# Performance work log

Hardware: AMD Instinct MI355X
Metric: run time of the kernel (lower is better)

The kernel has to match this reference:

```python
import jax, jax.numpy as jnp
import numpy as np

N = 65536      # n query/support points
NN = 34        # neighbors per point
K = 15         # kernel points
IN_F = 64
OUT_F = 64
RADIUS = 2.5
KP_EXTENT_CFG = 1.0
DENSITY = 5.0
EXTENT = KP_EXTENT_CFG * RADIUS / DENSITY  # effective KP_extent = 0.5
BN_EPS = 1e-6
LRELU_SLOPE = 0.1
POINT_DIM = 4  # modulated=True -> 3 offset dims + 1 modulation per kernel point


def make_kernel_points():
    # Deterministic stand-in for the precomputed kernel dispositions loaded
    # from disk in KPConv (fixed='center': first point at origin). Points lie
    # inside a ball of radius 1.5 * extent.
    rng = np.random.RandomState(42)
    kp = rng.normal(size=(K, 3))
    kp /= np.linalg.norm(kp, axis=1, keepdims=True)
    kp *= rng.uniform(0.3, 1.0, size=(K, 1))
    kp[0] = 0.0
    return jnp.asarray(kp * (1.5 * EXTENT), dtype=jnp.float32)


def setup_inputs() -> dict:
    key = jax.random.key(0)
    ks = jax.random.split(key, 8)
    query_points = jax.random.uniform(ks[0], (N, 3), dtype=jnp.float32)
    support_points = jax.random.uniform(ks[1], (N, 3), dtype=jnp.float32)
    neighbors_indices = jax.random.randint(ks[2], (N, NN), 0, N, dtype=jnp.int32)
    features = jax.random.normal(ks[3], (N, IN_F), dtype=jnp.float32)
    # weight_variable: truncated normal with std sqrt(2/size[-1])
    weight = jax.random.truncated_normal(ks[4], -2.0, 2.0, (K, IN_F, OUT_F), jnp.float32) * np.sqrt(2.0 / OUT_F)
    off_dim = POINT_DIM * K
    offset_weight = jax.random.truncated_normal(ks[5], -2.0, 2.0, (K, IN_F, off_dim), jnp.float32) * np.sqrt(2.0 / off_dim)
    offset_bias = jnp.zeros((off_dim,), jnp.float32)
    bn_gamma = jnp.ones((OUT_F,), jnp.float32)
    bn_beta = jnp.zeros((OUT_F,), jnp.float32)
    kernel_points = make_kernel_points()
    return dict(query_points=query_points, support_points=support_points,
                neighbors_indices=neighbors_indices, features=features,
                weight=weight, offset_weight=offset_weight, offset_bias=offset_bias,
                bn_gamma=bn_gamma, bn_beta=bn_beta, kernel_points=kernel_points)


def _influence(sq_dist):
    # KP_influence='linear': relu(1 - d / extent)
    return jax.nn.relu(1.0 - jnp.sqrt(sq_dist) / EXTENT)


def reference(query_points, support_points, neighbors_indices, features,
              weight, offset_weight, offset_bias, bn_gamma, bn_beta, kernel_points):
    n = query_points.shape[0]
    # Shadow point (far away) / shadow feature (zeros) appended at index n0
    supp_pad = jnp.concatenate([support_points, jnp.full((1, 3), 1e6, jnp.float32)], 0)
    feat_pad = jnp.concatenate([features, jnp.zeros((1, IN_F), jnp.float32)], 0)

    neigh_pts = supp_pad[neighbors_indices] - query_points[:, None, :]   # [n,nn,3]
    neigh_feats = feat_pad[neighbors_indices]                            # [n,nn,in]

    # ---- rigid KPConv producing per-point offsets (+ modulations) ----
    sq0 = jnp.sum((neigh_pts[:, :, None, :] - kernel_points[None, None]) ** 2, -1)  # [n,nn,K]
    w0 = _influence(sq0)
    wf0 = jnp.einsum('nak,nac->nkc', w0, neigh_feats)                    # [n,K,in]
    f0 = jnp.einsum('nkc,kcd->nd', wf0, offset_weight) + offset_bias     # [n,4K]
    offsets = f0[:, :3 * K].reshape(n, K, 3) * EXTENT                    # rescale to layer extent
    modulations = 2.0 * jax.nn.sigmoid(f0[:, 3 * K:])                    # [n,K]

    # ---- deformable KPConv ----
    def_kp = kernel_points[None] + offsets                               # [n,K,3]
    sq = jnp.sum((neigh_pts[:, :, None, :] - def_kp[:, None, :, :]) ** 2, -1)  # [n,nn,K]
    w = _influence(sq)                                                   # aggregation_mode='sum'
    wf = jnp.einsum('nak,nac->nkc', w, neigh_feats) * modulations[:, :, None]
    x = jnp.einsum('nkc,kco->no', wf, weight)                            # [n,out]

    # BatchNorm1d (training-mode batch stats, eps=1e-6) + LeakyReLU(0.1)
    mean = x.mean(0)
    var = x.var(0)
    x = (x - mean) * jax.lax.rsqrt(var + BN_EPS) * bn_gamma + bn_beta
    return jnp.where(x >= 0, x, LRELU_SLOPE * x)
```

## Files before the change

### kernel.cpp

```cpp
#include <hip/hip_runtime.h>
#include <math.h>

#define NPTS 65536

using half8   = __attribute__((ext_vector_type(8))) _Float16;
using half4   = __attribute__((ext_vector_type(4))) _Float16;
using floatx4 = __attribute__((ext_vector_type(4))) float;

__global__ __launch_bounds__(256) void k_prep(
    const float* __restrict__ ow, const float* __restrict__ w,
    const float* __restrict__ feat,
    _Float16* __restrict__ owt, _Float16* __restrict__ wt,
    _Float16* __restrict__ featH, float* __restrict__ stats)
{
  int b = blockIdx.x;
  if (b < 64) {
    __shared__ float tile[256][9];
    int mat = b >> 5, bb = b & 31;
    int kcb = bb & 3, db = bb >> 2;
    int t = threadIdx.x;
    int kc = kcb * 256 + t;
    int c = kc >> 4, k = kc & 15;
    const float* src = mat ? w : ow;
    int dmax = mat ? 64 : 60;
    #pragma unroll
    for (int di = 0; di < 8; ++di) {
      int d = db * 8 + di;
      float v = 0.f;
      if (k < 15 && d < dmax) v = src[(k * 64 + c) * dmax + d];
      tile[t][di] = v;
    }
    __syncthreads();
    _Float16* dst = mat ? wt : owt;
    int k2 = t >> 5, lo = t & 31;
    #pragma unroll
    for (int di = 0; di < 8; ++di) {
      int d = db * 8 + di;
      int wv = d >> 4, mm = d & 15;
      dst[((wv * 4 + kcb) * 8 + k2) * 512 + mm * 32 + lo] = (_Float16)tile[t][di];
    }
    if (b == 0 && t < 128) stats[t] = 0.f;
  } else {
    int j = (b - 64) * 256 + threadIdx.x;
    float4 f = ((const float4*)feat)[j];
    half4 h = {(_Float16)f.x, (_Float16)f.y, (_Float16)f.z, (_Float16)f.w};
    ((half4*)featH)[j] = h;
  }
}

__global__ __launch_bounds__(256, 4) void k_fused(
    const float* __restrict__ query, const float* __restrict__ support,
    const int* __restrict__ nidx, const _Float16* __restrict__ featH,
    const float* __restrict__ kpts, const float* __restrict__ obias,
    const _Float16* __restrict__ owt, const _Float16* __restrict__ wt,
    float* __restrict__ outx, float* __restrict__ stats)
{
  __shared__ float                  npx[16][34], npy[16][34], npz[16][34];
  __shared__ unsigned short         sidx[16][34];
  __shared__ __align__(16) _Float16 fT[4][64 * 32];
  __shared__ unsigned int           fx2s[16][64];
  __shared__ __align__(16) _Float16 wfh[16 * 264];
  __shared__ float                  dk[16][60];

  const int tid  = threadIdx.x;
  const int wave = tid >> 6, lane = tid & 63;
  const int quad = lane >> 4, mm = lane & 15;
  const int base = blockIdx.x * 16;
  _Float16* fTw = fT[wave];
  unsigned int* fTw32 = (unsigned int*)fTw;
  const floatx4 fz = {0.f, 0.f, 0.f, 0.f};
  const int me = (mm < 15) ? mm : 14;
  const int mmw = (mm & 6) | ((mm & 1) << 3) | ((mm >> 3) & 1);

  for (int s = tid; s < 544; s += 256) {
    int pt = s / 34, a = s - pt * 34;
    int n = base + pt;
    int id = nidx[n * 34 + a];
    npx[pt][a] = support[id * 3 + 0] - query[n * 3 + 0];
    npy[pt][a] = support[id * 3 + 1] - query[n * 3 + 1];
    npz[pt][a] = support[id * 3 + 2] - query[n * 3 + 2];
    sidx[pt][a] = (unsigned short)id;
  }
  __syncthreads();

  if (tid < 128) {
    int pt = tid >> 3, ch = tid & 7;
    int i0 = (int)sidx[pt][32], i1 = (int)sidx[pt][33];
    uint4 g0 = *(const uint4*)(featH + i0 * 64 + ch * 8);
    uint4 g1 = *(const uint4*)(featH + i1 * 64 + ch * 8);
    const uint* p0 = (const uint*)&g0;
    const uint* p1 = (const uint*)&g1;
    #pragma unroll
    for (int cc = 0; cc < 8; ++cc) {
      uint v = __builtin_amdgcn_perm(p1[cc >> 1], p0[cc >> 1],
                                     (cc & 1) ? 0x07060302u : 0x05040100u);
      fx2s[pt][ch * 8 + cc] = v;
    }
  }
  __syncthreads();

  auto load_g = [&](int pl, uint4* g0, uint4* g1) {
    #pragma unroll
    for (int it = 0; it < 2; ++it) {
      int task = it * 64 + lane;
      int rp = task >> 3, ch = task & 7;
      int i0 = (int)sidx[pl][2 * rp], i1 = (int)sidx[pl][2 * rp + 1];
      g0[it] = *(const uint4*)(featH + i0 * 64 + ch * 8);
      g1[it] = *(const uint4*)(featH + i1 * 64 + ch * 8);
    }
  };
  auto transpose_g = [&](const uint4* g0, const uint4* g1) {
    #pragma unroll
    for (int it = 0; it < 2; ++it) {
      int task = it * 64 + lane;
      int rp = task >> 3, ch = task & 7;
      int chunk = rp >> 2, o = rp & 3;
      const uint* p0 = (const uint*)&g0[it];
      const uint* p1 = (const uint*)&g1[it];
      #pragma unroll
      for (int cc = 0; cc < 8; ++cc) {
        int c  = ch * 8 + cc;
        int fc = (c & 0x36) | ((c & 1) << 3) | ((c >> 3) & 1);
        int pc = chunk ^ ((ch ^ cc) & 3);
        uint v = __builtin_amdgcn_perm(p1[cc >> 1], p0[cc >> 1],
                                       (cc & 1) ? 0x07060302u : 0x05040100u);
        fTw32[fc * 16 + pc * 4 + o] = v;
      }
    }
  };

  auto conv_point = [&](int pl, float kx, float ky, float kz, float modme,
                        half4* hq3) {
    half8 a0;
    #pragma unroll
    for (int j = 0; j < 8; ++j) {
      int a = quad * 8 + j;
      float dx = npx[pl][a] - kx, dy = npy[pl][a] - ky, dz = npz[pl][a] - kz;
      float wv = 1.f - 2.f * sqrtf(dx * dx + dy * dy + dz * dz);
      a0[j] = (_Float16)(fmaxf(wv, 0.f) * modme);
    }
    float dx = npx[pl][32] - kx, dy = npy[pl][32] - ky, dz = npz[pl][32] - kz;
    float w32 = fmaxf(1.f - 2.f * sqrtf(dx * dx + dy * dy + dz * dz), 0.f) * modme;
    dx = npx[pl][33] - kx; dy = npy[pl][33] - ky; dz = npz[pl][33] - kz;
    float w33 = fmaxf(1.f - 2.f * sqrtf(dx * dx + dy * dy + dz * dz), 0.f) * modme;
    half8 a2 = {};
    a2[0] = (_Float16)((quad == 0) ? w32 : 0.f);
    a2[1] = (_Float16)((quad == 0) ? w33 : 0.f);
    #pragma unroll
    for (int ct = 0; ct < 4; ++ct) {
      int c  = ct * 16 + mmw;
      int pc = quad ^ (((c >> 3) ^ c) & 3);
      half8 b = *(const half8*)(fTw + (ct * 16 + mm) * 32 + pc * 8);
      floatx4 acc = __builtin_amdgcn_mfma_f32_16x16x32_f16(a0, b, fz, 0, 0, 0);
      uint fp = fx2s[pl][c];
      half8 b2 = {};
      b2[0] = __builtin_bit_cast(_Float16, (unsigned short)(fp & 0xffffu));
      b2[1] = __builtin_bit_cast(_Float16, (unsigned short)(fp >> 16));
      acc = __builtin_amdgcn_mfma_f32_16x16x32_f16(a2, b2, acc, 0, 0, 0);
      half4 h = {(_Float16)acc[0], (_Float16)acc[1],
                 (_Float16)acc[2], (_Float16)acc[3]};
      if (ct == 0) *(half4*)(wfh + pl * 264 + mmw * 16 + quad * 4) = h;
      else         hq3[ct - 1] = h;
    }
  };

  auto write_hold = [&](const half4 (*hq)[3], int idx) {
    #pragma unroll
    for (int pp = 0; pp < 4; ++pp)
      *(half4*)(wfh + (wave * 4 + pp) * 264 + mmw * 16 + quad * 4) = hq[pp][idx];
  };

  auto gemm_q = [&](const _Float16* bmat, int p, floatx4& A, floatx4& B) {
    const _Float16* brow = bmat + ((wave * 4 + p) * 8) * 512 + mm * 32 + quad * 8;
    const _Float16* arow = wfh + mm * 264;
    #pragma unroll
    for (int k2 = 0; k2 < 8; ++k2) {
      half8 af = *(const half8*)(arow + k2 * 32 + quad * 8);
      half8 bf = *(const half8*)(brow + k2 * 512);
      if (k2 & 1) B = __builtin_amdgcn_mfma_f32_16x16x32_f16(af, bf, B, 0, 0, 0);
      else        A = __builtin_amdgcn_mfma_f32_16x16x32_f16(af, bf, A, 0, 0, 0);
    }
  };

  uint4 G0[2], G1[2];
  half4 hq[4][3];
  const float k0x = kpts[me * 3 + 0], k0y = kpts[me * 3 + 1], k0z = kpts[me * 3 + 2];

  {
    load_g(wave * 4, G0, G1);
    #pragma unroll
    for (int pp = 0; pp < 4; ++pp) {
      int pl = wave * 4 + pp;
      transpose_g(G0, G1);
      if (pp < 3) load_g(pl + 1, G0, G1);
      conv_point(pl, k0x, k0y, k0z, 1.f, hq[pp]);
    }
  }
  load_g(wave * 4, G0, G1);
  __syncthreads();

  {
    floatx4 A = fz, B = fz;
    gemm_q(owt, 0, A, B);
    __syncthreads(); write_hold(hq, 0); __syncthreads();
    gemm_q(owt, 1, A, B);
    __syncthreads(); write_hold(hq, 1); __syncthreads();
    gemm_q(owt, 2, A, B);
    __syncthreads(); write_hold(hq, 2); __syncthreads();
    gemm_q(owt, 3, A, B);
    int d = wave * 16 + mm;
    float bv = (d < 60) ? obias[d] : 0.f;
    float kv = (d < 45) ? kpts[d] : 0.f;
    #pragma unroll
    for (int r = 0; r < 4; ++r) {
      int pt = quad * 4 + r;
      float v = A[r] + B[r] + bv;
      if (d < 60)
        dk[pt][d] = (d < 45) ? (kv + 0.5f * v)
                             : (2.f / (1.f + expf(-v)));
    }
  }
  __syncthreads();

  #pragma unroll
  for (int pp = 0; pp < 4; ++pp) {
    int pl = wave * 4 + pp;
    float kx = dk[pl][me * 3 + 0], ky = dk[pl][me * 3 + 1], kz = dk[pl][me * 3 + 2];
    float modme = dk[pl][45 + me];
    transpose_g(G0, G1);
    if (pp < 3) load_g(pl + 1, G0, G1);
    conv_point(pl, kx, ky, kz, modme, hq[pp]);
  }
  __syncthreads();

  {
    floatx4 A = fz, B = fz;
    gemm_q(wt, 0, A, B);
    __syncthreads(); write_hold(hq, 0); __syncthreads();
    gemm_q(wt, 1, A, B);
    __syncthreads(); write_hold(hq, 1); __syncthreads();
    gemm_q(wt, 2, A, B);
    __syncthreads(); write_hold(hq, 2); __syncthreads();
    gemm_q(wt, 3, A, B);
    int d = wave * 16 + mm;
    float s1 = 0.f, s2 = 0.f;
    #pragma unroll
    for (int r = 0; r < 4; ++r) {
      float v = A[r] + B[r];
      outx[(base + quad * 4 + r) * 64 + d] = v;
      s1 += v; s2 += v * v;
    }
    s1 += __shfl_xor(s1, 16); s2 += __shfl_xor(s2, 16);
    s1 += __shfl_xor(s1, 32); s2 += __shfl_xor(s2, 32);
    if (lane < 16) {
      atomicAdd(&stats[d], s1);
      atomicAdd(&stats[64 + d], s2);
    }
  }
}

__global__ __launch_bounds__(256) void k_norm(
    float* __restrict__ x, const float* __restrict__ stats,
    const float* __restrict__ gamma, const float* __restrict__ beta)
{
  const int i = blockIdx.x * 256 + threadIdx.x;
  float4 v = ((float4*)x)[i];
  const int c0 = (i * 4) & 63;
  float o[4] = {v.x, v.y, v.z, v.w};
  #pragma unroll
  for (int j = 0; j < 4; ++j) {
    int c = c0 + j;
    float mean = stats[c] * (1.f / NPTS);
    float var  = stats[64 + c] * (1.f / NPTS) - mean * mean;
    float s = rsqrtf(var + 1e-6f) * gamma[c];
    float y = (o[j] - mean) * s + beta[c];
    o[j] = (y >= 0.f) ? y : 0.1f * y;
  }
  float4 rv = {o[0], o[1], o[2], o[3]};
  ((float4*)x)[i] = rv;
}

extern "C" void kernel_launch(void* const* d_in, const int* in_sizes, int n_in,
                              void* d_out, int out_size, void* d_ws, size_t ws_size,
                              hipStream_t stream)
{
  const float* query   = (const float*)d_in[0];
  const float* support = (const float*)d_in[1];
  const int*   nidx    = (const int*)d_in[2];
  const float* feat    = (const float*)d_in[3];
  const float* weight  = (const float*)d_in[4];
  const float* oweight = (const float*)d_in[5];
  const float* obias   = (const float*)d_in[6];
  const float* gamma   = (const float*)d_in[7];
  const float* beta    = (const float*)d_in[8];
  const float* kpts    = (const float*)d_in[9];
  float* x = (float*)d_out;

  char* ws = (char*)d_ws;
  _Float16* featH = (_Float16*)ws;
  _Float16* owt   = (_Float16*)(ws + 8388608);
  _Float16* wt    = (_Float16*)(ws + 8519680);
  float*    stats = (float*)(ws + 8650752);

  k_prep<<<4160, 256, 0, stream>>>(oweight, weight, feat, owt, wt, featH, stats);
  k_fused<<<4096, 256, 0, stream>>>(query, support, nidx, featH, kpts, obias,
                                    owt, wt, x, stats);
  k_norm<<<4096, 256, 0, stream>>>(x, stats, gamma, beta);
}
```

Baseline: 257.0 us.

## Pack neighbor offsets as float4 with squared norm and expand distance algebraically

Neighbor offsets now go into one float4 array that also holds the precomputed squared norm. Kernel-point distances are computed as |p|^2+|k|^2-2p·k, which replaces per-pair subtractions with a dot product and turns three LDS reads into one vector read. The deformed kernel points and modulations are stored in fp16 in shared memory, and the MFMA loops in gemm_q raise wave priority with s_setprio. The expanded form risks cancellation error and the fp16 offsets lose precision, though the distance is clamped at zero.

```diff
diff --git a/kernel.cpp b/kernel.cpp
--- a/kernel.cpp
+++ b/kernel.cpp
@@ -55,12 +55,12 @@
     const _Float16* __restrict__ owt, const _Float16* __restrict__ wt,
     float* __restrict__ outx, float* __restrict__ stats)
 {
-  __shared__ float                  npx[16][34], npy[16][34], npz[16][34];
+  __shared__ float4                 np4[16][34];
   __shared__ unsigned short         sidx[16][34];
   __shared__ __align__(16) _Float16 fT[4][64 * 32];
   __shared__ unsigned int           fx2s[16][64];
   __shared__ __align__(16) _Float16 wfh[16 * 264];
-  __shared__ float                  dk[16][60];
+  __shared__ _Float16               dkh[16][60];
 
   const int tid  = threadIdx.x;
   const int wave = tid >> 6, lane = tid & 63;
@@ -76,9 +76,11 @@
     int pt = s / 34, a = s - pt * 34;
     int n = base + pt;
     int id = nidx[n * 34 + a];
-    npx[pt][a] = support[id * 3 + 0] - query[n * 3 + 0];
-    npy[pt][a] = support[id * 3 + 1] - query[n * 3 + 1];
-    npz[pt][a] = support[id * 3 + 2] - query[n * 3 + 2];
+    float dx = support[id * 3 + 0] - query[n * 3 + 0];
+    float dy = support[id * 3 + 1] - query[n * 3 + 1];
+    float dz = support[id * 3 + 2] - query[n * 3 + 2];
+    float4 q = {dx, dy, dz, dx * dx + dy * dy + dz * dz};
+    np4[pt][a] = q;
     sidx[pt][a] = (unsigned short)id;
   }
   __syncthreads();
@@ -131,18 +133,22 @@
 
   auto conv_point = [&](int pl, float kx, float ky, float kz, float modme,
                         half4* hq3) {
+    float hk = kx * kx + ky * ky + kz * kz;
     half8 a0;
     #pragma unroll
     for (int j = 0; j < 8; ++j) {
       int a = quad * 8 + j;
-      float dx = npx[pl][a] - kx, dy = npy[pl][a] - ky, dz = npz[pl][a] - kz;
-      float wv = 1.f - 2.f * sqrtf(dx * dx + dy * dy + dz * dz);
-      a0[j] = (_Float16)(fmaxf(wv, 0.f) * modme);
-    }
-    float dx = npx[pl][32] - kx, dy = npy[pl][32] - ky, dz = npz[pl][32] - kz;
-    float w32 = fmaxf(1.f - 2.f * sqrtf(dx * dx + dy * dy + dz * dz), 0.f) * modme;
-    dx = npx[pl][33] - kx; dy = npy[pl][33] - ky; dz = npz[pl][33] - kz;
-    float w33 = fmaxf(1.f - 2.f * sqrtf(dx * dx + dy * dy + dz * dz), 0.f) * modme;
+      float4 q = np4[pl][a];
+      float dt = q.x * kx + q.y * ky + q.z * kz;
+      float d2 = fmaxf(q.w + hk - 2.f * dt, 0.f);
+      a0[j] = (_Float16)(fmaxf(1.f - 2.f * sqrtf(d2), 0.f) * modme);
+    }
+    float4 q = np4[pl][32];
+    float dt = q.x * kx + q.y * ky + q.z * kz;
+    float w32 = fmaxf(1.f - 2.f * sqrtf(fmaxf(q.w + hk - 2.f * dt, 0.f)), 0.f) * modme;
+    q = np4[pl][33];
+    dt = q.x * kx + q.y * ky + q.z * kz;
+    float w33 = fmaxf(1.f - 2.f * sqrtf(fmaxf(q.w + hk - 2.f * dt, 0.f)), 0.f) * modme;
     half8 a2 = {};
     a2[0] = (_Float16)((quad == 0) ? w32 : 0.f);
     a2[1] = (_Float16)((quad == 0) ? w33 : 0.f);
@@ -173,6 +179,7 @@
   auto gemm_q = [&](const _Float16* bmat, int p, floatx4& A, floatx4& B) {
     const _Float16* brow = bmat + ((wave * 4 + p) * 8) * 512 + mm * 32 + quad * 8;
     const _Float16* arow = wfh + mm * 264;
+    __builtin_amdgcn_s_setprio(1);
     #pragma unroll
     for (int k2 = 0; k2 < 8; ++k2) {
       half8 af = *(const half8*)(arow + k2 * 32 + quad * 8);
@@ -180,6 +187,7 @@
       if (k2 & 1) B = __builtin_amdgcn_mfma_f32_16x16x32_f16(af, bf, B, 0, 0, 0);
       else        A = __builtin_amdgcn_mfma_f32_16x16x32_f16(af, bf, A, 0, 0, 0);
     }
+    __builtin_amdgcn_s_setprio(0);
   };
 
   uint4 G0[2], G1[2];
@@ -216,8 +224,8 @@
       int pt = quad * 4 + r;
       float v = A[r] + B[r] + bv;
       if (d < 60)
-        dk[pt][d] = (d < 45) ? (kv + 0.5f * v)
-                             : (2.f / (1.f + expf(-v)));
+        dkh[pt][d] = (_Float16)((d < 45) ? (kv + 0.5f * v)
+                                         : (2.f / (1.f + expf(-v))));
     }
   }
   __syncthreads();
@@ -225,8 +233,10 @@
   #pragma unroll
   for (int pp = 0; pp < 4; ++pp) {
     int pl = wave * 4 + pp;
-    float kx = dk[pl][me * 3 + 0], ky = dk[pl][me * 3 + 1], kz = dk[pl][me * 3 + 2];
-    float modme = dk[pl][45 + me];
+    float kx = (float)dkh[pl][me * 3 + 0];
+    float ky = (float)dkh[pl][me * 3 + 1];
+    float kz = (float)dkh[pl][me * 3 + 2];
+    float modme = (float)dkh[pl][45 + me];
     transpose_g(G0, G1);
     if (pp < 3) load_g(pl + 1, G0, G1);
     conv_point(pl, kx, ky, kz, modme, hq[pp]);
```

After: 254.0 us. Within noise of the previous version (-1.1%).
